# Performance work log

Measured on AMD Instinct MI355X. Metric: run time of the kernel, lower is better.

The kernel has to match this reference:

```python
import jax, jax.numpy as jnp
import numpy as np

L = 16
B = 128
_PERM = np.array([0, 6, 2, 4, 3, 5, 1, 7])  # stabilizer swap permutation


def _swap_stabilizers(t):
    # t: (b, L, L, L, 8, 2, 2, 2). Torch does permute(0,4,3,2,1) on (N,8,2,2,2)
    # rows, i.e. reverse the trailing 4 dims, reshape back, then permute dim -4.
    shape = t.shape
    t = jnp.transpose(t, (0, 1, 2, 3, 7, 6, 5, 4)).reshape(shape)
    return t[:, :, :, :, _PERM]


def _surface_to_flags(surf):
    # surf: (..., L) int. flip, roll 1, cumsum, roll 1, parity.
    s = jnp.flip(surf, axis=-1)
    s = jnp.roll(s, 1, axis=-1)
    c = jnp.roll(jnp.cumsum(s, axis=-1), 1, axis=-1)
    return (c % 2) > 0


def _get_z_flag(syn_str, axis, shift, l):
    b = syn_str.shape[0]
    syn = syn_str.reshape(b, l, l, l)
    r = jnp.roll(syn, shift, axis=3 - axis)
    surf = jnp.sum(r, axis=1 + axis)  # (b, l, l)
    return _surface_to_flags(surf)


def _get_x_flag(syn_str, axis, shift, l):
    b = syn_str.shape[0]
    syn = syn_str.reshape(b, l, l, l)
    r = jnp.roll(syn, shift, axis=3 - axis)
    surf = jnp.sum(r, axis=(1 + axis, 1 + (1 + axis) % 3))  # (b, l)
    return _surface_to_flags(surf)


def _logic_action_average(probs, syndrome, axis, l):
    b = probs.shape[0]
    z_syn, x0, x1, x2 = jnp.split(syndrome, 4, axis=1)
    x_ch = (x0, x1, x2)[axis]

    # --- Z (dual lattice) update ---
    fz = _get_z_flag(z_syn, axis=axis, shift=0, l=l)  # (b, l, l)
    # torch: fz.unsqueeze(-1).repeat(1,1,1,l).permute(0,3,2,1)
    # => mask[b,i,j,k] = fz[b,k,j]
    mask_z = jnp.broadcast_to(jnp.transpose(fz, (0, 2, 1))[:, None], (b, l, l, l))
    cand = _swap_stabilizers(probs)
    cand = jnp.roll(cand, 1, axis=-3 + axis)  # roll one of the trailing 2-dims
    cand = _swap_stabilizers(cand)
    probs = jnp.where(mask_z[..., None, None, None, None], cand, probs)

    # --- X (primal lattice) update ---
    fx = _get_x_flag(x_ch, axis=axis, shift=1, l=l)  # (b, l)
    # torch: fx[...,None,None].repeat(1,1,l,l).permute(0,3,2,1)
    # => mask[b,i,j,k] = fx[b,k]
    mask_x = jnp.broadcast_to(fx[:, None, None, :], (b, l, l, l))
    rolled = jnp.roll(probs, 1, axis=-1 - axis)
    probs = jnp.where(mask_x[..., None, None, None, None], rolled, probs)
    return probs


def setup_inputs() -> dict:
    key = jax.random.key(0)
    k1, k2 = jax.random.split(key)
    x = jax.random.uniform(k1, (B, L, L, L, 8, 2, 2, 2), dtype=jnp.float32)
    syndrome = jax.random.randint(k2, (B, 4 * L ** 3), 0, 2, dtype=jnp.int32)
    return {"x": x, "syndrome": syndrome}


def reference(x, syndrome) -> jnp.ndarray:
    l = L
    for axis in range(3):
        x = _logic_action_average(x, syndrome, axis, l)
        x = jnp.transpose(x, (0, 2, 3, 1, 4, 5, 6, 7))
    return jnp.mean(x, axis=(1, 2, 3))  # (b, 8, 2, 2, 2)
```

## Files before the change

kernel.cpp:

```cpp
#include <hip/hip_runtime.h>
#include <stdint.h>

#define BATCH 128

#define OFF_FZ0 0
#define OFF_FZ1 (OFF_FZ0 + BATCH * 256)
#define OFF_FZ2 (OFF_FZ1 + BATCH * 256)
#define OFF_FX0 (OFF_FZ2 + BATCH * 256)
#define OFF_FX1 (OFF_FX0 + BATCH * 16)
#define OFF_FX2 (OFF_FX1 + BATCH * 16)

__device__ __forceinline__ int A_of(int o) {
    return ((o & 7) << 3) | (((o >> 3) & 1) << 2) | (((o >> 4) & 1) << 1) | ((o >> 5) & 1);
}
__device__ __forceinline__ int S_of(int o) {
    const unsigned P = (0u) | (6u << 3) | (2u << 6) | (4u << 9) | (3u << 12) |
                       (5u << 15) | (1u << 18) | (7u << 21);
    int s = (int)((P >> (3 * (o >> 3))) & 7u);
    return A_of((s << 3) | (o & 7));
}

__device__ __forceinline__ unsigned flag16(const unsigned char* r, int pos) {
    unsigned f;
    if (pos == 0) {
        f = 0;
#pragma unroll
        for (int w = 0; w < 16; ++w) f ^= r[w];
    } else {
        f = r[0];
        for (int w = 17 - pos; w <= 15; ++w) f ^= r[w];
    }
    return f & 1u;
}

__global__ __launch_bounds__(256) void k_flags(const int* __restrict__ syn,
                                               unsigned char* __restrict__ ws) {
    int b = blockIdx.x;
    int t = threadIdx.x;
    const int* base = syn + (size_t)b * 16384;
    const int* z  = base;
    const int* x0 = base + 4096;
    const int* x1 = base + 8192;
    const int* x2 = base + 12288;

    __shared__ unsigned char sp0[256], sp1[256], sp2[256];
    __shared__ unsigned char tA[256], tB[256], tC[256];
    __shared__ unsigned char g0[16], g1[16], g2[16];

    int dhi = t >> 4, dlo = t & 15;
    unsigned p;
    p = 0; for (int d1 = 0; d1 < 16; ++d1) p ^= (unsigned)z[d1 * 256 + t];            sp0[t] = p & 1;
    p = 0; for (int d2 = 0; d2 < 16; ++d2) p ^= (unsigned)z[dhi * 256 + d2 * 16 + dlo]; sp1[t] = p & 1;
    p = 0; for (int d3 = 0; d3 < 16; ++d3) p ^= (unsigned)z[dhi * 256 + dlo * 16 + d3]; sp2[t] = p & 1;
    p = 0; for (int d1 = 0; d1 < 16; ++d1) p ^= (unsigned)x0[d1 * 256 + t];           tA[t] = p & 1;
    p = 0; for (int d3 = 0; d3 < 16; ++d3) p ^= (unsigned)x1[dhi * 256 + dlo * 16 + d3]; tB[t] = p & 1;
    p = 0; for (int d3 = 0; d3 < 16; ++d3) p ^= (unsigned)x2[dhi * 256 + dlo * 16 + d3]; tC[t] = p & 1;
    __syncthreads();

    if (t < 16) {
        unsigned q = 0;
        for (int d2 = 0; d2 < 16; ++d2) q ^= tA[d2 * 16 + t];
        g0[(t + 1) & 15] = q & 1;
    } else if (t < 32) {
        int d1 = t - 16; unsigned q = 0;
        for (int d2 = 0; d2 < 16; ++d2) q ^= tB[d1 * 16 + d2];
        g1[d1] = q & 1;
    } else if (t < 48) {
        int d2 = t - 32; unsigned q = 0;
        for (int d1 = 0; d1 < 16; ++d1) q ^= tC[d1 * 16 + d2];
        g2[d2] = q & 1;
    }
    __syncthreads();

    ws[OFF_FZ0 + b * 256 + t] = (unsigned char)flag16(&sp0[dhi * 16], dlo);
    ws[OFF_FZ1 + b * 256 + t] = (unsigned char)flag16(&sp1[dhi * 16], dlo);
    ws[OFF_FZ2 + b * 256 + t] = (unsigned char)flag16(&sp2[dhi * 16], dlo);
    if (t < 16) {
        ws[OFF_FX0 + b * 16 + t] = (unsigned char)flag16(g0, t);
        ws[OFF_FX1 + b * 16 + t] = (unsigned char)flag16(g1, t);
        ws[OFF_FX2 + b * 16 + t] = (unsigned char)flag16(g2, t);
    }
}

__global__ __launch_bounds__(256) void k_main(const float* __restrict__ x,
                                              const unsigned char* __restrict__ ws,
                                              float* __restrict__ out) {
    __shared__ unsigned char T[4096];
    __shared__ unsigned char fz0[256], fz1[256], fz2[256];
    __shared__ unsigned char fx0[16], fx1[16], fx2[16];
    __shared__ unsigned char mArr[256];
    __shared__ unsigned char Ctab[3][64];
    __shared__ float red[256];

    int b  = blockIdx.y;
    int i0 = blockIdx.x;
    int t  = threadIdx.x;

    fz0[t] = ws[OFF_FZ0 + b * 256 + t];
    fz1[t] = ws[OFF_FZ1 + b * 256 + t];
    fz2[t] = ws[OFF_FZ2 + b * 256 + t];
    if (t < 16) {
        fx0[t] = ws[OFF_FX0 + b * 16 + t];
        fx1[t] = ws[OFF_FX1 + b * 16 + t];
        fx2[t] = ws[OFF_FX2 + b * 16 + t];
    }
    if (t < 192) {
        int ax = t >> 6, o = t & 63;
        int bit = 4 >> ax;
        Ctab[ax][o] = (unsigned char)S_of(S_of(o) ^ bit);
    }
    __syncthreads();

    {
        int j0 = t >> 4, k0 = t & 15;
        unsigned m = (unsigned)fz0[k0 * 16 + j0]
                   | ((unsigned)fx0[k0] << 1)
                   | ((unsigned)fz1[i0 * 16 + k0] << 2)
                   | ((unsigned)fx1[i0] << 3)
                   | ((unsigned)fz2[j0 * 16 + i0] << 4)
                   | ((unsigned)fx2[j0] << 5);
        mArr[t] = (unsigned char)m;
    }
    for (int idx = t; idx < 4096; idx += 256) {
        int m = idx >> 6, v = idx & 63;
        int src = v;
        if (m & 32) src ^= 4;
        if (m & 16) src = Ctab[2][src];
        if (m & 8)  src ^= 2;
        if (m & 4)  src = Ctab[1][src];
        if (m & 2)  src ^= 1;
        if (m & 1)  src = Ctab[0][src];
        T[idx] = (unsigned char)src;
    }
    __syncthreads();

    int wave = t >> 6, v = t & 63;
    const float* xb = x + (((size_t)b * 4096 + (size_t)i0 * 256) << 6);
    float acc = 0.f;
#pragma unroll 4
    for (int it = 0; it < 64; ++it) {
        int sl = wave * 64 + it;
        float val = xb[((size_t)sl << 6) + v];
        int m   = mArr[sl];
        int src = T[(m << 6) | v];
        int pulled = __builtin_amdgcn_ds_bpermute(src << 2, __float_as_int(val));
        acc += __int_as_float(pulled);
    }
    red[t] = acc;
    __syncthreads();
    if (t < 64) {
        float s4 = red[t] + red[t + 64] + red[t + 128] + red[t + 192];
        atomicAdd(out + b * 64 + t, s4 * (1.0f / 4096.0f));
    }
}

extern "C" void kernel_launch(void* const* d_in, const int* in_sizes, int n_in,
                              void* d_out, int out_size, void* d_ws, size_t ws_size,
                              hipStream_t stream) {
    const float* x   = (const float*)d_in[0];
    const int*   syn = (const int*)d_in[1];
    float* out = (float*)d_out;
    unsigned char* ws = (unsigned char*)d_ws;

    hipMemsetAsync(d_out, 0, (size_t)out_size * sizeof(float), stream);
    k_flags<<<BATCH, 256, 0, stream>>>(syn, ws);
    k_main<<<dim3(16, BATCH), 256, 0, stream>>>(x, ws, out);
}
```

Before: 203.0 us.

## Split flag kernel into per-job blocks and double-buffer x via LDS DMA

The flag kernel now launches six blocks per batch, one per flag job, instead of one block computing all six serially. This adds parallelism to a small, latency-bound kernel. The main kernel replaces direct global loads plus a ds_bpermute gather with global_load_lds 16-byte DMA into a double-buffered 32 KB LDS tile. The gather then becomes an LDS read at the permuted index. This adds LDS pressure and block-wide barriers per chunk, and relies on the compiler inserting correct waitcnts for the async LDS loads.

```diff
diff --git a/kernel.cpp b/kernel.cpp
--- a/kernel.cpp
+++ b/kernel.cpp
@@ -35,56 +35,86 @@
 
 __global__ __launch_bounds__(256) void k_flags(const int* __restrict__ syn,
                                                unsigned char* __restrict__ ws) {
-    int b = blockIdx.x;
-    int t = threadIdx.x;
+    int b = blockIdx.x, job = blockIdx.y, t = threadIdx.x;
+    int dhi = t >> 4, dlo = t & 15;
     const int* base = syn + (size_t)b * 16384;
-    const int* z  = base;
-    const int* x0 = base + 4096;
-    const int* x1 = base + 8192;
-    const int* x2 = base + 12288;
-
-    __shared__ unsigned char sp0[256], sp1[256], sp2[256];
-    __shared__ unsigned char tA[256], tB[256], tC[256];
-    __shared__ unsigned char g0[16], g1[16], g2[16];
-
-    int dhi = t >> 4, dlo = t & 15;
-    unsigned p;
-    p = 0; for (int d1 = 0; d1 < 16; ++d1) p ^= (unsigned)z[d1 * 256 + t];            sp0[t] = p & 1;
-    p = 0; for (int d2 = 0; d2 < 16; ++d2) p ^= (unsigned)z[dhi * 256 + d2 * 16 + dlo]; sp1[t] = p & 1;
-    p = 0; for (int d3 = 0; d3 < 16; ++d3) p ^= (unsigned)z[dhi * 256 + dlo * 16 + d3]; sp2[t] = p & 1;
-    p = 0; for (int d1 = 0; d1 < 16; ++d1) p ^= (unsigned)x0[d1 * 256 + t];           tA[t] = p & 1;
-    p = 0; for (int d3 = 0; d3 < 16; ++d3) p ^= (unsigned)x1[dhi * 256 + dlo * 16 + d3]; tB[t] = p & 1;
-    p = 0; for (int d3 = 0; d3 < 16; ++d3) p ^= (unsigned)x2[dhi * 256 + dlo * 16 + d3]; tC[t] = p & 1;
-    __syncthreads();
-
-    if (t < 16) {
-        unsigned q = 0;
-        for (int d2 = 0; d2 < 16; ++d2) q ^= tA[d2 * 16 + t];
-        g0[(t + 1) & 15] = q & 1;
-    } else if (t < 32) {
-        int d1 = t - 16; unsigned q = 0;
-        for (int d2 = 0; d2 < 16; ++d2) q ^= tB[d1 * 16 + d2];
-        g1[d1] = q & 1;
-    } else if (t < 48) {
-        int d2 = t - 32; unsigned q = 0;
-        for (int d1 = 0; d1 < 16; ++d1) q ^= tC[d1 * 16 + d2];
-        g2[d2] = q & 1;
-    }
-    __syncthreads();
-
-    ws[OFF_FZ0 + b * 256 + t] = (unsigned char)flag16(&sp0[dhi * 16], dlo);
-    ws[OFF_FZ1 + b * 256 + t] = (unsigned char)flag16(&sp1[dhi * 16], dlo);
-    ws[OFF_FZ2 + b * 256 + t] = (unsigned char)flag16(&sp2[dhi * 16], dlo);
-    if (t < 16) {
-        ws[OFF_FX0 + b * 16 + t] = (unsigned char)flag16(g0, t);
-        ws[OFF_FX1 + b * 16 + t] = (unsigned char)flag16(g1, t);
-        ws[OFF_FX2 + b * 16 + t] = (unsigned char)flag16(g2, t);
-    }
+    __shared__ unsigned char sp[256];
+    __shared__ unsigned char g[16];
+    unsigned p = 0;
+
+    if (job == 0) {
+        const int* z = base;
+#pragma unroll
+        for (int d1 = 0; d1 < 16; ++d1) p ^= (unsigned)z[d1 * 256 + t];
+        sp[t] = p & 1;
+        __syncthreads();
+        ws[OFF_FZ0 + b * 256 + t] = (unsigned char)flag16(&sp[dhi * 16], dlo);
+    } else if (job == 1) {
+        const int* z = base;
+#pragma unroll
+        for (int d2 = 0; d2 < 16; ++d2) p ^= (unsigned)z[dhi * 256 + d2 * 16 + dlo];
+        sp[t] = p & 1;
+        __syncthreads();
+        ws[OFF_FZ1 + b * 256 + t] = (unsigned char)flag16(&sp[dhi * 16], dlo);
+    } else if (job == 2) {
+        const int* z = base;
+#pragma unroll
+        for (int d3 = 0; d3 < 16; ++d3) p ^= (unsigned)z[dhi * 256 + dlo * 16 + d3];
+        sp[t] = p & 1;
+        __syncthreads();
+        ws[OFF_FZ2 + b * 256 + t] = (unsigned char)flag16(&sp[dhi * 16], dlo);
+    } else if (job == 3) {
+        const int* x0 = base + 4096;
+#pragma unroll
+        for (int d1 = 0; d1 < 16; ++d1) p ^= (unsigned)x0[d1 * 256 + t];
+        sp[t] = p & 1;
+        __syncthreads();
+        if (t < 16) {
+            unsigned q = 0;
+            for (int d2 = 0; d2 < 16; ++d2) q ^= sp[d2 * 16 + t];
+            g[(t + 1) & 15] = q & 1;
+        }
+        __syncthreads();
+        if (t < 16) ws[OFF_FX0 + b * 16 + t] = (unsigned char)flag16(g, t);
+    } else if (job == 4) {
+        const int* x1 = base + 8192;
+#pragma unroll
+        for (int d3 = 0; d3 < 16; ++d3) p ^= (unsigned)x1[dhi * 256 + dlo * 16 + d3];
+        sp[t] = p & 1;
+        __syncthreads();
+        if (t < 16) {
+            unsigned q = 0;
+            for (int d2 = 0; d2 < 16; ++d2) q ^= sp[t * 16 + d2];
+            g[t] = q & 1;
+        }
+        __syncthreads();
+        if (t < 16) ws[OFF_FX1 + b * 16 + t] = (unsigned char)flag16(g, t);
+    } else {
+        const int* x2 = base + 12288;
+#pragma unroll
+        for (int d3 = 0; d3 < 16; ++d3) p ^= (unsigned)x2[dhi * 256 + dlo * 16 + d3];
+        sp[t] = p & 1;
+        __syncthreads();
+        if (t < 16) {
+            unsigned q = 0;
+            for (int d1 = 0; d1 < 16; ++d1) q ^= sp[d1 * 16 + t];
+            g[t] = q & 1;
+        }
+        __syncthreads();
+        if (t < 16) ws[OFF_FX2 + b * 16 + t] = (unsigned char)flag16(g, t);
+    }
+}
+
+typedef const __attribute__((address_space(1))) uint32_t glob_u32;
+typedef __attribute__((address_space(3))) uint32_t lds_u32;
+__device__ __forceinline__ void dma16(const float* g, float* l) {
+    __builtin_amdgcn_global_load_lds((glob_u32*)g, (lds_u32*)l, 16, 0, 0);
 }
 
 __global__ __launch_bounds__(256) void k_main(const float* __restrict__ x,
                                               const unsigned char* __restrict__ ws,
                                               float* __restrict__ out) {
+    __shared__ float buf[2][64 * 64];
     __shared__ unsigned char T[4096];
     __shared__ unsigned char fz0[256], fz1[256], fz2[256];
     __shared__ unsigned char fx0[16], fx1[16], fx2[16];
@@ -95,6 +125,18 @@
     int b  = blockIdx.y;
     int i0 = blockIdx.x;
     int t  = threadIdx.x;
+    int w  = t >> 6, v = t & 63;
+
+    const float* xb = x + (((size_t)b * 4096 + (size_t)i0 * 256) << 6);
+
+    {
+        const float* gsrc = xb + ((w * 16) << 6) + (v << 2);
+        float* ldst = &buf[0][(w * 16) << 6];
+        dma16(gsrc,       ldst);
+        dma16(gsrc + 256, ldst + 256);
+        dma16(gsrc + 512, ldst + 512);
+        dma16(gsrc + 768, ldst + 768);
+    }
 
     fz0[t] = ws[OFF_FZ0 + b * 256 + t];
     fz1[t] = ws[OFF_FZ1 + b * 256 + t];
@@ -122,8 +164,8 @@
         mArr[t] = (unsigned char)m;
     }
     for (int idx = t; idx < 4096; idx += 256) {
-        int m = idx >> 6, v = idx & 63;
-        int src = v;
+        int m = idx >> 6, vv = idx & 63;
+        int src = vv;
         if (m & 32) src ^= 4;
         if (m & 16) src = Ctab[2][src];
         if (m & 8)  src ^= 2;
@@ -134,18 +176,29 @@
     }
     __syncthreads();
 
-    int wave = t >> 6, v = t & 63;
-    const float* xb = x + (((size_t)b * 4096 + (size_t)i0 * 256) << 6);
     float acc = 0.f;
-#pragma unroll 4
-    for (int it = 0; it < 64; ++it) {
-        int sl = wave * 64 + it;
-        float val = xb[((size_t)sl << 6) + v];
-        int m   = mArr[sl];
-        int src = T[(m << 6) | v];
-        int pulled = __builtin_amdgcn_ds_bpermute(src << 2, __float_as_int(val));
-        acc += __int_as_float(pulled);
-    }
+    const unsigned char* Trow = T;
+#pragma unroll
+    for (int c = 0; c < 4; ++c) {
+        if (c < 3) {
+            const float* gsrc = xb + (((c + 1) * 64 + w * 16) << 6) + (v << 2);
+            float* ldst = &buf[(c + 1) & 1][(w * 16) << 6];
+            dma16(gsrc,       ldst);
+            dma16(gsrc + 256, ldst + 256);
+            dma16(gsrc + 512, ldst + 512);
+            dma16(gsrc + 768, ldst + 768);
+        }
+        const float* bufw = &buf[c & 1][(w * 16) << 6];
+        int sl_base = c * 64 + w * 16;
+#pragma unroll
+        for (int it = 0; it < 16; ++it) {
+            int m   = mArr[sl_base + it];
+            int src = Trow[(m << 6) | v];
+            acc += bufw[(it << 6) | src];
+        }
+        __syncthreads();
+    }
+
     red[t] = acc;
     __syncthreads();
     if (t < 64) {
@@ -163,6 +216,6 @@
     unsigned char* ws = (unsigned char*)d_ws;
 
     hipMemsetAsync(d_out, 0, (size_t)out_size * sizeof(float), stream);
-    k_flags<<<BATCH, 256, 0, stream>>>(syn, ws);
+    k_flags<<<dim3(BATCH, 6), 256, 0, stream>>>(syn, ws);
     k_main<<<dim3(16, BATCH), 256, 0, stream>>>(x, ws, out);
 }
```

Measured after the change: 199.2 us. About the same (-1.8%).
